# Kernel tuning notes

Hardware: AMD Instinct MI355X
Metric: run time of the kernel (lower is better)

Reference implementation:

```python
import jax, jax.numpy as jnp
import numpy as np

NUM_EMBEDDINGS = 1024
EMBEDDING_DIM = 64
COMMITMENT_COST = 0.25


def setup_inputs() -> dict:
    key = jax.random.key(0)
    k1, k2 = jax.random.split(key)
    latents = jax.random.normal(k1, (64, EMBEDDING_DIM, 32, 32), dtype=jnp.float32)
    # torch init: uniform_(-1/num_embeddings, 1/num_embeddings)
    codebook = jax.random.uniform(
        k2, (NUM_EMBEDDINGS, EMBEDDING_DIM), dtype=jnp.float32,
        minval=-1.0 / NUM_EMBEDDINGS, maxval=1.0 / NUM_EMBEDDINGS)
    return {"latents": latents, "codebook": codebook}


def reference(latents, codebook):
    B, C, H, W = latents.shape
    K = codebook.shape[0]
    x = jnp.transpose(latents, (0, 2, 3, 1))            # [B,H,W,C]
    x_flat = x.reshape(-1, C)                            # [N,C]
    # squared euclidean distances [N,K]
    dist = (jnp.sum(x_flat ** 2, axis=1, keepdims=True)
            + jnp.sum(codebook ** 2, axis=1)
            - 2.0 * x_flat @ codebook.T)
    idx = jnp.argmin(dist, axis=1)                       # [N] int
    q_flat = codebook[idx]                               # [N,C]
    q = q_flat.reshape(x.shape)                          # [B,H,W,C]
    e_loss = jnp.mean((jax.lax.stop_gradient(q) - x) ** 2)
    q_loss = jnp.mean((q - jax.lax.stop_gradient(x)) ** 2)
    vq_loss = q_loss + COMMITMENT_COST * e_loss
    # straight-through estimator
    q_st = x + jax.lax.stop_gradient(q - x)
    quantized = jnp.transpose(q_st, (0, 3, 1, 2))        # [B,C,H,W]
    # perplexity from code usage histogram
    N = x_flat.shape[0]
    avg_probs = jnp.zeros((K,), dtype=jnp.float32).at[idx].add(1.0) / N
    perplexity = jnp.exp(-jnp.sum(avg_probs * jnp.log(avg_probs + 1e-10)))
    encoding_indices = idx.reshape(B, H, W)
    return (vq_loss, quantized, perplexity, encoding_indices)
```

## Files before the change

### kernel.cpp

```cpp
#include <hip/hip_runtime.h>

#define N_PTS   65536
#define K_CODES 1024
#define C_DIM   64
#define HW      1024
#define Q_ELEMS 4194304

#define OUT_Q_OFF 1
#define OUT_P_OFF 4194305
#define OUT_I_OFF 4194306

#define WS_HIST 0
#define WS_SSE  4096
#define WS_DONE 4104
#define WS_CSUM 8192
#define WS_CBP  16384

#define EPS_A_W 7.5e-5f
#define EPS_T_W 2.0e-4f

typedef float f32x16 __attribute__((ext_vector_type(16)));
typedef short bf16x8 __attribute__((ext_vector_type(8)));

__device__ __forceinline__ unsigned short bf16rn(float f) {
    unsigned int u = __float_as_uint(f);
    return (unsigned short)((u + 0x7FFFu + ((u >> 16) & 1u)) >> 16);
}
__device__ __forceinline__ float bf16tof(unsigned short h) {
    return __uint_as_float(((unsigned int)h) << 16);
}

__device__ __forceinline__ void gload_lds16(const void* g, void* l) {
    __builtin_amdgcn_global_load_lds(
        (const __attribute__((address_space(1))) unsigned int*)g,
        (__attribute__((address_space(3))) unsigned int*)l, 16, 0, 0);
}

__device__ __forceinline__ float np_pairwise_sumsq64(const float* a) {
    float r[8];
    #pragma unroll
    for (int j = 0; j < 8; ++j) r[j] = __fmul_rn(a[j], a[j]);
    #pragma unroll
    for (int i = 8; i < 64; i += 8) {
        #pragma unroll
        for (int j = 0; j < 8; ++j)
            r[j] = __fadd_rn(r[j], __fmul_rn(a[i + j], a[i + j]));
    }
    return __fadd_rn(__fadd_rn(__fadd_rn(r[0], r[1]), __fadd_rn(r[2], r[3])),
                     __fadd_rn(__fadd_rn(r[4], r[5]), __fadd_rn(r[6], r[7])));
}

__global__ void vq_prep(const float* __restrict__ cb, float* __restrict__ csum,
                        unsigned short* __restrict__ cbp,
                        unsigned int* __restrict__ hist,
                        double* __restrict__ sse,
                        unsigned int* __restrict__ done) {
    int g = blockIdx.x * 256 + threadIdx.x;
    if (g < 1024) hist[g] = 0u;
    if (g == 1024) { *sse = 0.0; *done = 0u; }
    int t = g >> 6, lane = g & 63, l31 = lane & 31, half = lane >> 5;
    int row = t * 32 + l31;
    const float* r = cb + row * 64;
    float cs = np_pairwise_sumsq64(r);
    if (half == 0) csum[row] = cs;
    size_t tb = (size_t)t * 4096;
    #pragma unroll
    for (int c = 0; c < 4; ++c) {
        bf16x8 h8, l8;
        #pragma unroll
        for (int j = 0; j < 8; ++j) {
            float f = r[c * 16 + half * 8 + j];
            unsigned short h = bf16rn(f);
            h8[j] = (short)h;
            l8[j] = (short)bf16rn(f - bf16tof(h));
        }
        *(bf16x8*)(cbp + tb + (size_t)(c * 2 + 0) * 512 + lane * 8) = h8;
        *(bf16x8*)(cbp + tb + (size_t)(c * 2 + 1) * 512 + lane * 8) = l8;
    }
}

__global__ __launch_bounds__(256, 1) void vq_main(
        const float* __restrict__ latents,
        const float* __restrict__ cb,
        const float* __restrict__ csum,
        const unsigned short* __restrict__ cbp,
        unsigned int* __restrict__ hist,
        double* __restrict__ sse,
        unsigned int* __restrict__ done,
        float* __restrict__ out) {
    __shared__ float xs[128 * 65];
    __shared__ float tmax[32 * 128];
    __shared__ float csl[1024];
    __shared__ __align__(16) short stg[2][2048];
    __shared__ float m1f[128];
    __shared__ int   fk[128], ambig[128], acount;
    __shared__ double wred[4];
    __shared__ int isLast;

    const int tid  = threadIdx.x;
    const int lane = tid & 63, wave = tid >> 6;
    const int n0 = blockIdx.x * 128;
    const int b = n0 >> 10, hw0 = n0 & 1023;
    const float* xg = latents + (size_t)b * C_DIM * HW + hw0;

    for (int i = tid; i < 128 * 64; i += 256) {
        int p = i & 127, d = i >> 7;
        xs[p * 65 + d] = xg[(size_t)d * HW + p];
    }
    for (int i = tid; i < 1024; i += 256) csl[i] = -0.5f * csum[i];
    if (tid == 0) acount = 0;
    __syncthreads();

    const int l31 = lane & 31, half = lane >> 5;
    const int pb = (wave << 5) + l31;
    bf16x8 xh[4], xl[4];
    #pragma unroll
    for (int c = 0; c < 4; ++c)
        #pragma unroll
        for (int j = 0; j < 8; ++j) {
            float f = xs[pb * 65 + c * 16 + half * 8 + j];
            unsigned short h = bf16rn(f);
            xh[c][j] = (short)h;
            xl[c][j] = (short)bf16rn(f - bf16tof(h));
        }

    f32x16 zacc;
    #pragma unroll
    for (int r = 0; r < 16; ++r) zacc[r] = 0.0f;

    float m1 = -3e38f, m2 = -3e38f;
    int i1 = 0;
    const int RC[16] = {0,1,2,3,8,9,10,11,16,17,18,19,24,25,26,27};
    const int rh4 = half * 4;
    const char* cbpB = (const char*)cbp;
    char* lds0 = (char*)&stg[0][0] + wave * 1024;
    char* lds1 = (char*)&stg[1][0] + wave * 1024;

    gload_lds16(cbpB + (size_t)tid * 16, lds0);

    for (int t = 0; t < 32; ++t) {
        __syncthreads();
        const bf16x8* s0 = (const bf16x8*)&stg[0][0];
        bf16x8 a0 = s0[lane], a1 = s0[64 + lane], a2 = s0[128 + lane], a3 = s0[192 + lane];
        f32x16 csv;
        {
            const int cb0 = (t << 5) + rh4;
            #pragma unroll
            for (int q = 0; q < 4; ++q) {
                float4 c4 = *(const float4*)&csl[cb0 + q * 8];
                csv[q * 4 + 0] = c4.x; csv[q * 4 + 1] = c4.y;
                csv[q * 4 + 2] = c4.z; csv[q * 4 + 3] = c4.w;
            }
        }
        gload_lds16(cbpB + ((size_t)(2 * t + 1)) * 4096 + (size_t)tid * 16, lds1);
        f32x16 acc0 = __builtin_amdgcn_mfma_f32_32x32x16_bf16(a0, xh[0], csv, 0, 0, 0);
        acc0 = __builtin_amdgcn_mfma_f32_32x32x16_bf16(a0, xl[0], acc0, 0, 0, 0);
        acc0 = __builtin_amdgcn_mfma_f32_32x32x16_bf16(a1, xh[0], acc0, 0, 0, 0);
        acc0 = __builtin_amdgcn_mfma_f32_32x32x16_bf16(a2, xh[1], acc0, 0, 0, 0);
        acc0 = __builtin_amdgcn_mfma_f32_32x32x16_bf16(a2, xl[1], acc0, 0, 0, 0);
        acc0 = __builtin_amdgcn_mfma_f32_32x32x16_bf16(a3, xh[1], acc0, 0, 0, 0);

        __syncthreads();
        const bf16x8* s1 = (const bf16x8*)&stg[1][0];
        bf16x8 b0 = s1[lane], b1 = s1[64 + lane], b2 = s1[128 + lane], b3 = s1[192 + lane];
        if (t < 31)
            gload_lds16(cbpB + ((size_t)(2 * t + 2)) * 4096 + (size_t)tid * 16, lds0);
        f32x16 acc1 = __builtin_amdgcn_mfma_f32_32x32x16_bf16(b0, xh[2], zacc, 0, 0, 0);
        acc1 = __builtin_amdgcn_mfma_f32_32x32x16_bf16(b0, xl[2], acc1, 0, 0, 0);
        acc1 = __builtin_amdgcn_mfma_f32_32x32x16_bf16(b1, xh[2], acc1, 0, 0, 0);
        acc1 = __builtin_amdgcn_mfma_f32_32x32x16_bf16(b2, xh[3], acc1, 0, 0, 0);
        acc1 = __builtin_amdgcn_mfma_f32_32x32x16_bf16(b2, xl[3], acc1, 0, 0, 0);
        acc1 = __builtin_amdgcn_mfma_f32_32x32x16_bf16(b3, xh[3], acc1, 0, 0, 0);

        float vl = -3e38f, sl = -3e38f;
        int kl = 0;
        #pragma unroll
        for (int r = 0; r < 16; ++r) {
            float v = acc0[r] + acc1[r];
            sl = __builtin_amdgcn_fmed3f(v, sl, vl);
            bool c2 = v > vl;
            kl = c2 ? RC[r] : kl;
            vl = fmaxf(vl, v);
        }
        int k = (t << 5) + rh4 + kl;
        bool cg = vl > m1;
        i1 = cg ? k : i1;
        float X = cg ? sl : m2;
        m2 = __builtin_amdgcn_fmed3f(vl, X, m1);
        m1 = fmaxf(m1, vl);
        float tlm = fmaxf(vl, __shfl_xor(vl, 32, 64));
        if (half == 0) tmax[t * 128 + pb] = tlm;
    }

    {
        float m1o = __shfl_xor(m1, 32, 64);
        float m2o = __shfl_xor(m2, 32, 64);
        int   i1o = __shfl_xor(i1, 32, 64);
        m2 = fmaxf(fmaxf(m2, m2o), fminf(m1, m1o));
        i1 = (m1o > m1) ? i1o : i1;
        m1 = fmaxf(m1, m1o);
        if (half == 0) {
            m1f[pb] = m1;
            fk[pb] = i1;
            if (m2 >= m1 - EPS_A_W) {
                int a = atomicAdd(&acount, 1);
                ambig[a] = pb;
            }
        }
    }
    __syncthreads();

    for (int a = wave; a < acount; a += 4) {
        int p = ambig[a];
        const float* xrow = &xs[p * 65];
        float Aq = np_pairwise_sumsq64(xrow);
        float thr = m1f[p] - EPS_T_W;
        unsigned long long best = ~0ULL;
        for (int t = 0; t < 32; ++t) {
            if (tmax[t * 128 + p] < thr) continue;
            if (lane < 32) {
                int k = (t << 5) + lane;
                const float* crow = cb + (size_t)k * 64;
                float m = 0.0f;
                #pragma unroll
                for (int d = 0; d < 64; ++d) m = __fmaf_rn(xrow[d], crow[d], m);
                float D = __fsub_rn(__fadd_rn(Aq, csum[k]), __fmul_rn(2.0f, m));
                unsigned long long key =
                    ((unsigned long long)__float_as_uint(D) << 10) | (unsigned)k;
                best = (key < best) ? key : best;
            }
        }
        #pragma unroll
        for (int off = 32; off > 0; off >>= 1) {
            unsigned long long o = __shfl_xor(best, off, 64);
            best = (o < best) ? o : best;
        }
        if (lane == 0) fk[p] = (int)(best & 1023ULL);
    }
    __syncthreads();

    if (tid < 128) {
        int myk = fk[tid];
        out[OUT_I_OFF + n0 + tid] = (float)myk;
        atomicAdd(&hist[myk], 1u);
    }
    double e = 0.0;
    #pragma unroll
    for (int i2 = 0; i2 < 8; ++i2) {
        int i = tid + i2 * 256;
        int p = i >> 4, seg = i & 15;
        const float4 q = *(const float4*)(cb + (size_t)fk[p] * 64 + seg * 4);
        float* xp = &xs[p * 65 + seg * 4];
        float x0 = xp[0], x1 = xp[1], x2 = xp[2], x3 = xp[3];
        double d0 = (double)x0 - (double)q.x; e = fma(d0, d0, e);
        double d1 = (double)x1 - (double)q.y; e = fma(d1, d1, e);
        double d2 = (double)x2 - (double)q.z; e = fma(d2, d2, e);
        double d3 = (double)x3 - (double)q.w; e = fma(d3, d3, e);
        xp[0] = q.x; xp[1] = q.y; xp[2] = q.z; xp[3] = q.w;
    }
    #pragma unroll
    for (int off = 32; off > 0; off >>= 1) e += __shfl_down(e, off, 64);
    if (lane == 0) wred[wave] = e;
    __syncthreads();
    if (tid == 0) {
        double s = 0.0;
        #pragma unroll
        for (int w = 0; w < 4; ++w) s += wred[w];
        atomicAdd(sse, s);
    }
    for (int i = tid; i < 128 * 64; i += 256) {
        int p = i & 127, c = i >> 7;
        out[OUT_Q_OFF + (size_t)b * 65536 + (size_t)c * HW + hw0 + p] = xs[p * 65 + c];
    }

    __syncthreads();
    if (tid == 0)
        isLast = (atomicAdd(done, 1u) == (unsigned)(gridDim.x - 1)) ? 1 : 0;
    __syncthreads();
    if (isLast) {
        double s = 0.0;
        for (int i = tid; i < K_CODES; i += 256) {
            unsigned int h = __hip_atomic_load(&hist[i], __ATOMIC_RELAXED,
                                               __HIP_MEMORY_SCOPE_AGENT);
            double pr = (double)h / (double)N_PTS;
            s += pr * log(pr + 1e-10);
        }
        #pragma unroll
        for (int off = 32; off > 0; off >>= 1) s += __shfl_down(s, off, 64);
        if (lane == 0) wred[wave] = s;
        __syncthreads();
        if (tid == 0) {
            double st = 0.0;
            #pragma unroll
            for (int w = 0; w < 4; ++w) st += wred[w];
            double sv = __hip_atomic_load(sse, __ATOMIC_RELAXED,
                                          __HIP_MEMORY_SCOPE_AGENT);
            out[OUT_P_OFF] = (float)exp(-st);
            out[0] = (float)(1.25 * sv / (double)Q_ELEMS);
        }
    }
}

extern "C" void kernel_launch(void* const* d_in, const int* in_sizes, int n_in,
                              void* d_out, int out_size, void* d_ws, size_t ws_size,
                              hipStream_t stream) {
    const float* latents = (const float*)d_in[0];
    const float* cb      = (const float*)d_in[1];
    float* out = (float*)d_out;
    char* ws = (char*)d_ws;

    unsigned int*   hist = (unsigned int*)(ws + WS_HIST);
    double*         sse  = (double*)(ws + WS_SSE);
    unsigned int*   done = (unsigned int*)(ws + WS_DONE);
    float*          csum = (float*)(ws + WS_CSUM);
    unsigned short* cbp  = (unsigned short*)(ws + WS_CBP);

    vq_prep<<<8, 256, 0, stream>>>(cb, csum, cbp, hist, sse, done);
    vq_main<<<N_PTS / 128, 256, 0, stream>>>(latents, cb, csum, cbp,
                                             hist, sse, done, out);
}
```

Baseline: 133.8 us.

## Merge codebook staging into one barrier per tile and interleave MFMA chains

The per-iteration staging of the packed codebook now uses one 8 KB double-buffered slab per tile instead of two 4 KB halves, each behind its own barrier. This halves the number of block-wide __syncthreads in the main loop. The two independent MFMA accumulation chains are interleaved to hide MFMA dependency latency. The per-tile max table is stored as bf16, with a conservative upward bound applied when read back, which frees LDS for the larger staging buffers; in exchange the rescan may visit slightly more tiles.

```diff
diff --git a/kernel.cpp b/kernel.cpp
--- a/kernel.cpp
+++ b/kernel.cpp
@@ -89,9 +89,9 @@
         unsigned int* __restrict__ done,
         float* __restrict__ out) {
     __shared__ float xs[128 * 65];
-    __shared__ float tmax[32 * 128];
+    __shared__ unsigned short tmaxh[32 * 128];
     __shared__ float csl[1024];
-    __shared__ __align__(16) short stg[2][2048];
+    __shared__ __align__(16) short stg[2][4096];
     __shared__ float m1f[128];
     __shared__ int   fk[128], ambig[128], acount;
     __shared__ double wred[4];
@@ -133,15 +133,25 @@
     const int RC[16] = {0,1,2,3,8,9,10,11,16,17,18,19,24,25,26,27};
     const int rh4 = half * 4;
     const char* cbpB = (const char*)cbp;
-    char* lds0 = (char*)&stg[0][0] + wave * 1024;
-    char* lds1 = (char*)&stg[1][0] + wave * 1024;
-
-    gload_lds16(cbpB + (size_t)tid * 16, lds0);
+    char* buf0 = (char*)&stg[0][0] + wave * 1024;
+    char* buf1 = (char*)&stg[1][0] + wave * 1024;
+
+    gload_lds16(cbpB + (size_t)tid * 16, buf0);
+    gload_lds16(cbpB + 4096 + (size_t)tid * 16, buf0 + 4096);
 
     for (int t = 0; t < 32; ++t) {
         __syncthreads();
-        const bf16x8* s0 = (const bf16x8*)&stg[0][0];
-        bf16x8 a0 = s0[lane], a1 = s0[64 + lane], a2 = s0[128 + lane], a3 = s0[192 + lane];
+        char* nxt = (t & 1) ? buf0 : buf1;
+        if (t + 1 < 32) {
+            const char* src = cbpB + ((size_t)(t + 1)) * 8192 + (size_t)tid * 16;
+            gload_lds16(src, nxt);
+            gload_lds16(src + 4096, nxt + 4096);
+        }
+        const bf16x8* s = (const bf16x8*)((t & 1) ? &stg[1][0] : &stg[0][0]);
+        bf16x8 h0 = s[0 * 64 + lane], o0 = s[1 * 64 + lane];
+        bf16x8 h1 = s[2 * 64 + lane], o1 = s[3 * 64 + lane];
+        bf16x8 h2 = s[4 * 64 + lane], o2 = s[5 * 64 + lane];
+        bf16x8 h3 = s[6 * 64 + lane], o3 = s[7 * 64 + lane];
         f32x16 csv;
         {
             const int cb0 = (t << 5) + rh4;
@@ -152,25 +162,18 @@
                 csv[q * 4 + 2] = c4.z; csv[q * 4 + 3] = c4.w;
             }
         }
-        gload_lds16(cbpB + ((size_t)(2 * t + 1)) * 4096 + (size_t)tid * 16, lds1);
-        f32x16 acc0 = __builtin_amdgcn_mfma_f32_32x32x16_bf16(a0, xh[0], csv, 0, 0, 0);
-        acc0 = __builtin_amdgcn_mfma_f32_32x32x16_bf16(a0, xl[0], acc0, 0, 0, 0);
-        acc0 = __builtin_amdgcn_mfma_f32_32x32x16_bf16(a1, xh[0], acc0, 0, 0, 0);
-        acc0 = __builtin_amdgcn_mfma_f32_32x32x16_bf16(a2, xh[1], acc0, 0, 0, 0);
-        acc0 = __builtin_amdgcn_mfma_f32_32x32x16_bf16(a2, xl[1], acc0, 0, 0, 0);
-        acc0 = __builtin_amdgcn_mfma_f32_32x32x16_bf16(a3, xh[1], acc0, 0, 0, 0);
-
-        __syncthreads();
-        const bf16x8* s1 = (const bf16x8*)&stg[1][0];
-        bf16x8 b0 = s1[lane], b1 = s1[64 + lane], b2 = s1[128 + lane], b3 = s1[192 + lane];
-        if (t < 31)
-            gload_lds16(cbpB + ((size_t)(2 * t + 2)) * 4096 + (size_t)tid * 16, lds0);
-        f32x16 acc1 = __builtin_amdgcn_mfma_f32_32x32x16_bf16(b0, xh[2], zacc, 0, 0, 0);
-        acc1 = __builtin_amdgcn_mfma_f32_32x32x16_bf16(b0, xl[2], acc1, 0, 0, 0);
-        acc1 = __builtin_amdgcn_mfma_f32_32x32x16_bf16(b1, xh[2], acc1, 0, 0, 0);
-        acc1 = __builtin_amdgcn_mfma_f32_32x32x16_bf16(b2, xh[3], acc1, 0, 0, 0);
-        acc1 = __builtin_amdgcn_mfma_f32_32x32x16_bf16(b2, xl[3], acc1, 0, 0, 0);
-        acc1 = __builtin_amdgcn_mfma_f32_32x32x16_bf16(b3, xh[3], acc1, 0, 0, 0);
+        f32x16 acc0 = __builtin_amdgcn_mfma_f32_32x32x16_bf16(h0, xh[0], csv, 0, 0, 0);
+        f32x16 acc1 = __builtin_amdgcn_mfma_f32_32x32x16_bf16(h2, xh[2], zacc, 0, 0, 0);
+        acc0 = __builtin_amdgcn_mfma_f32_32x32x16_bf16(h0, xl[0], acc0, 0, 0, 0);
+        acc1 = __builtin_amdgcn_mfma_f32_32x32x16_bf16(h2, xl[2], acc1, 0, 0, 0);
+        acc0 = __builtin_amdgcn_mfma_f32_32x32x16_bf16(o0, xh[0], acc0, 0, 0, 0);
+        acc1 = __builtin_amdgcn_mfma_f32_32x32x16_bf16(o2, xh[2], acc1, 0, 0, 0);
+        acc0 = __builtin_amdgcn_mfma_f32_32x32x16_bf16(h1, xh[1], acc0, 0, 0, 0);
+        acc1 = __builtin_amdgcn_mfma_f32_32x32x16_bf16(h3, xh[3], acc1, 0, 0, 0);
+        acc0 = __builtin_amdgcn_mfma_f32_32x32x16_bf16(h1, xl[1], acc0, 0, 0, 0);
+        acc1 = __builtin_amdgcn_mfma_f32_32x32x16_bf16(h3, xl[3], acc1, 0, 0, 0);
+        acc0 = __builtin_amdgcn_mfma_f32_32x32x16_bf16(o1, xh[1], acc0, 0, 0, 0);
+        acc1 = __builtin_amdgcn_mfma_f32_32x32x16_bf16(o3, xh[3], acc1, 0, 0, 0);
 
         float vl = -3e38f, sl = -3e38f;
         int kl = 0;
@@ -189,7 +192,7 @@
         m2 = __builtin_amdgcn_fmed3f(vl, X, m1);
         m1 = fmaxf(m1, vl);
         float tlm = fmaxf(vl, __shfl_xor(vl, 32, 64));
-        if (half == 0) tmax[t * 128 + pb] = tlm;
+        if (half == 0) tmaxh[t * 128 + pb] = bf16rn(tlm);
     }
 
     {
@@ -217,7 +220,8 @@
         float thr = m1f[p] - EPS_T_W;
         unsigned long long best = ~0ULL;
         for (int t = 0; t < 32; ++t) {
-            if (tmax[t * 128 + p] < thr) continue;
+            float tm = bf16tof(tmaxh[t * 128 + p]);
+            if (__fmaf_rn(fabsf(tm), 0x1p-8f, tm) < thr) continue;
             if (lane < 32) {
                 int k = (t << 5) + lane;
                 const float* crow = cb + (size_t)k * 64;
```

Result: faster. 127.0 us (-5.1%).
